# Kernel optimization log

Hardware: AMD Instinct MI355X
Metric: run time of the kernel (lower is better)

The kernel has to match this reference:

```python
import jax, jax.numpy as jnp
import numpy as np

M_DIM = 1024
N_HEADS = 16
H_DIM = M_DIM // N_HEADS
B, S_DEC, S_ENC = 2, 2048, 2048
NEG = -1e9
LN_EPS = 1e-5


def _layernorm(x, g, b):
    mu = jnp.mean(x, axis=-1, keepdims=True)
    var = jnp.mean(jnp.square(x - mu), axis=-1, keepdims=True)
    return (x - mu) * jax.lax.rsqrt(var + LN_EPS) * g + b


def _mha(q_in, kv_in, Wq, bq, Wk, bk, Wv, bv, causal):
    # Wq/Wk/Wv: [H, m_dim, h_dim]; stacked equivalent of per-head nn.Linear
    q = jnp.einsum('bsm,hmd->bhsd', q_in, Wq) + bq[:, None, :]
    k = jnp.einsum('bsm,hmd->bhsd', kv_in, Wk) + bk[:, None, :]
    v = jnp.einsum('bsm,hmd->bhsd', kv_in, Wv) + bv[:, None, :]
    scores = jnp.einsum('bhqd,bhkd->bhqk', q, k) / jnp.sqrt(jnp.asarray(H_DIM, q.dtype))
    if causal:
        sq, sk = scores.shape[-2], scores.shape[-1]
        mask = jnp.tril(jnp.ones((sq, sk), dtype=bool))
        scores = jnp.where(mask, scores, jnp.asarray(NEG, scores.dtype))
    attn = jax.nn.softmax(scores, axis=-1)
    o = jnp.einsum('bhqk,bhkd->bhqd', attn, v)
    bsz, h, sq, d = o.shape
    # concat order: head-major along last dim, same as torch.cat over heads
    return o.transpose(0, 2, 1, 3).reshape(bsz, sq, h * d)


def setup_inputs() -> dict:
    key = jax.random.key(0)
    ks = jax.random.split(key, 32)
    s = 1.0 / np.sqrt(M_DIM)
    s2 = 1.0 / np.sqrt(2 * M_DIM)
    d = {
        'input': jax.random.normal(ks[0], (B, S_DEC, M_DIM), jnp.float32),
        'encoder_out': jax.random.normal(ks[1], (B, S_ENC, M_DIM), jnp.float32),
        # self-attention heads (stacked)
        'Wq1': jax.random.normal(ks[2], (N_HEADS, M_DIM, H_DIM), jnp.float32) * s,
        'bq1': jnp.zeros((N_HEADS, H_DIM), jnp.float32),
        'Wk1': jax.random.normal(ks[3], (N_HEADS, M_DIM, H_DIM), jnp.float32) * s,
        'bk1': jnp.zeros((N_HEADS, H_DIM), jnp.float32),
        'Wv1': jax.random.normal(ks[4], (N_HEADS, M_DIM, H_DIM), jnp.float32) * s,
        'bv1': jnp.zeros((N_HEADS, H_DIM), jnp.float32),
        'Wo1': jax.random.normal(ks[5], (M_DIM, M_DIM), jnp.float32) * s,
        'bo1': jnp.zeros((M_DIM,), jnp.float32),
        'ln1_g': jnp.ones((M_DIM,), jnp.float32),
        'ln1_b': jnp.zeros((M_DIM,), jnp.float32),
        # cross-attention heads (stacked)
        'Wq2': jax.random.normal(ks[6], (N_HEADS, M_DIM, H_DIM), jnp.float32) * s,
        'bq2': jnp.zeros((N_HEADS, H_DIM), jnp.float32),
        'Wk2': jax.random.normal(ks[7], (N_HEADS, M_DIM, H_DIM), jnp.float32) * s,
        'bk2': jnp.zeros((N_HEADS, H_DIM), jnp.float32),
        'Wv2': jax.random.normal(ks[8], (N_HEADS, M_DIM, H_DIM), jnp.float32) * s,
        'bv2': jnp.zeros((N_HEADS, H_DIM), jnp.float32),
        'Wo2': jax.random.normal(ks[9], (M_DIM, M_DIM), jnp.float32) * s,
        'bo2': jnp.zeros((M_DIM,), jnp.float32),
        'ln2_g': jnp.ones((M_DIM,), jnp.float32),
        'ln2_b': jnp.zeros((M_DIM,), jnp.float32),
        # FFN (expansion factor 2, per source)
        'W_ff1': jax.random.normal(ks[10], (M_DIM, 2 * M_DIM), jnp.float32) * s,
        'b_ff1': jnp.zeros((2 * M_DIM,), jnp.float32),
        'W_ff2': jax.random.normal(ks[11], (2 * M_DIM, M_DIM), jnp.float32) * s2,
        'b_ff2': jnp.zeros((M_DIM,), jnp.float32),
        'ln3_g': jnp.ones((M_DIM,), jnp.float32),
        'ln3_b': jnp.zeros((M_DIM,), jnp.float32),
    }
    return d


def reference(input, encoder_out,
              Wq1, bq1, Wk1, bk1, Wv1, bv1, Wo1, bo1, ln1_g, ln1_b,
              Wq2, bq2, Wk2, bk2, Wv2, bv2, Wo2, bo2, ln2_g, ln2_b,
              W_ff1, b_ff1, W_ff2, b_ff2, ln3_g, ln3_b):
    # masked self-attention (dropout = identity in eval)
    sa = _mha(input, input, Wq1, bq1, Wk1, bk1, Wv1, bv1, causal=True)
    sa = sa @ Wo1 + bo1
    out1 = _layernorm(sa + input, ln1_g, ln1_b)
    # cross-attention
    ca = _mha(out1, encoder_out, Wq2, bq2, Wk2, bk2, Wv2, bv2, causal=False)
    ca = ca @ Wo2 + bo2
    out1 = _layernorm(out1 + ca, ln2_g, ln2_b)
    # FFN
    ff = jax.nn.relu(out1 @ W_ff1 + b_ff1) @ W_ff2 + b_ff2
    out = _layernorm(ff + out1, ln3_g, ln3_b)
    return out
```

## Files before the change

### kernel.cpp

```cpp
#include <hip/hip_runtime.h>
#include <math.h>

#define B_ 2
#define S_ 2048
#define M_ 1024
#define H_ 16
#define D_ 64
#define R_ (B_*S_)

typedef __attribute__((ext_vector_type(8))) short short8v;
typedef __attribute__((ext_vector_type(4))) float float4v;
typedef __attribute__((ext_vector_type(16))) float float16v;

__device__ __forceinline__ float4 ld4(const float* p) {
    return *(const float4* __restrict__)p;
}

__device__ __forceinline__ ushort f2bf(float f) {
    union { float f; unsigned u; } x; x.f = f;
    unsigned u = x.u + 0x7fffu + ((x.u >> 16) & 1u);
    return (ushort)(u >> 16);
}
__device__ __forceinline__ float bf2f(ushort s) {
    union { unsigned u; float f; } x; x.u = ((unsigned)s) << 16; return x.f;
}
__device__ __forceinline__ unsigned cvtpk(float lo, float hi) {
    unsigned r;
    asm("v_cvt_pk_bf16_f32 %0, %1, %2" : "=v"(r) : "v"(lo), "v"(hi));
    return r;
}
#if __has_builtin(__builtin_amdgcn_exp2f)
__device__ __forceinline__ float fexp2(float x) { return __builtin_amdgcn_exp2f(x); }
#else
__device__ __forceinline__ float fexp2(float x) { return exp2f(x); }
#endif
#if __has_builtin(__builtin_amdgcn_rcpf)
__device__ __forceinline__ float frcp(float x) { return __builtin_amdgcn_rcpf(x); }
#else
__device__ __forceinline__ float frcp(float x) { return 1.f / x; }
#endif
__device__ __forceinline__ float4v mfma16(short8v a, short8v b, float4v c) {
    return __builtin_amdgcn_mfma_f32_16x16x32_bf16(a, b, c, 0, 0, 0);
}
__device__ __forceinline__ float16v mfma32(short8v a, short8v b, float16v c) {
    return __builtin_amdgcn_mfma_f32_32x32x16_bf16(a, b, c, 0, 0, 0);
}
__device__ __forceinline__ void glds16(const void* g, void* l) {
    __builtin_amdgcn_global_load_lds(
        (const __attribute__((address_space(1))) void*)g,
        (__attribute__((address_space(3))) void*)l, 16, 0, 0);
}

__global__ __launch_bounds__(256) void cast2_k(const float* __restrict__ a,
                                               const float* __restrict__ b,
                                               ushort* __restrict__ oa,
                                               ushort* __restrict__ ob) {
    size_t u = (size_t)blockIdx.x * 256 + threadIdx.x;
    const float* in; ushort* out;
    if (u < (1u << 20)) { in = a; out = oa; }
    else { u -= (1u << 20); in = b; out = ob; }
    float4 v = ld4(in + u * 4);
    ushort4 o = { f2bf(v.x), f2bf(v.y), f2bf(v.z), f2bf(v.w) };
    *(ushort4*)&out[u * 4] = o;
}

__global__ __launch_bounds__(256) void biasp_k(
    const float* __restrict__ q1, const float* __restrict__ k1,
    const float* __restrict__ v1, const float* __restrict__ k2,
    const float* __restrict__ v2, const float* __restrict__ q2,
    float* __restrict__ dst, float SCv) {
    const int seg = blockIdx.x >> 2;
    const int li = (blockIdx.x & 3) * 256 + threadIdx.x;
    const float* s; int off; float sc;
    switch (seg) {
        case 0: s = q1; off = 0;    sc = SCv; break;
        case 1: s = k1; off = 1024; sc = 1.f; break;
        case 2: s = v1; off = 2048; sc = 1.f; break;
        case 3: s = k2; off = 4096; sc = 1.f; break;
        case 4: s = v2; off = 5120; sc = 1.f; break;
        default: s = q2; off = 8192; sc = SCv; break;
    }
    dst[off + li] = s[li] * sc;
}

__global__ __launch_bounds__(256) void wtransH_k(
    const float* __restrict__ s0, const float* __restrict__ s1,
    const float* __restrict__ s2, const float* __restrict__ s3,
    const float* __restrict__ s4, const float* __restrict__ s5,
    ushort* __restrict__ oQKV1, ushort* __restrict__ oQ2,
    ushort* __restrict__ oKV2, float SCv) {
    __shared__ float t[32][33];
    const int z = blockIdx.z, s6 = z >> 4, h = z & 15;
    const float* srcs[6] = { s0, s1, s2, s3, s4, s5 };
    const float* ib = srcs[s6] + (size_t)h * 1024 * 64;
    ushort* ob;
    if (s6 < 3)       ob = oQKV1 + (size_t)s6 * (1024 * 1024) + (size_t)h * (64 * 1024);
    else if (s6 == 3) ob = oQ2 + (size_t)h * (64 * 1024);
    else              ob = oKV2 + (size_t)(s6 - 4) * (1024 * 1024) + (size_t)h * (64 * 1024);
    const float scale = (s6 == 0 || s6 == 3) ? SCv : 1.f;
    const int k0 = blockIdx.y * 32, n0 = blockIdx.x * 32;
    const int tx = threadIdx.x & 31, ty = threadIdx.x >> 5;
    #pragma unroll
    for (int i = 0; i < 4; ++i)
        t[ty + i * 8][tx] = ib[(size_t)(k0 + ty + i * 8) * 64 + n0 + tx];
    __syncthreads();
    #pragma unroll
    for (int i = 0; i < 4; ++i)
        ob[(size_t)(n0 + ty + i * 8) * 1024 + k0 + tx] = f2bf(t[tx][ty + i * 8] * scale);
}

__global__ __launch_bounds__(256) void wtrans_k(const float* __restrict__ inA,
                                                const float* __restrict__ inB,
                                                ushort* __restrict__ outA,
                                                ushort* __restrict__ outB,
                                                int K, int N) {
    __shared__ float t[32][33];
    const float* ib = blockIdx.z ? inB : inA;
    ushort* ob = blockIdx.z ? outB : outA;
    const int k0 = blockIdx.y * 32, n0 = blockIdx.x * 32;
    const int tx = threadIdx.x & 31, ty = threadIdx.x >> 5;
    #pragma unroll
    for (int i = 0; i < 4; ++i)
        t[ty + i * 8][tx] = ib[(size_t)(k0 + ty + i * 8) * N + n0 + tx];
    __syncthreads();
    #pragma unroll
    for (int i = 0; i < 4; ++i)
        ob[(size_t)(n0 + ty + i * 8) * K + k0 + tx] = f2bf(t[tx][ty + i * 8]);
}

template<int TM, int TN, int BK, int OUTMODE, int ACT>
__global__ __launch_bounds__(256) void gemm_bf16_k(
    const ushort* __restrict__ A, const ushort* __restrict__ Bt,
    const float* __restrict__ bias, void* __restrict__ C,
    ushort* __restrict__ Cvt, int matV, int N, int K)
{
    constexpr int NI = TM / 32;
    constexpr int NJ = TN / 32;
    constexpr int KS = BK / 32;
    constexpr int CHR = BK / 8;
    __shared__ __align__(16) ushort At[TM * BK];
    __shared__ __align__(16) ushort Bts[TN * BK];
    const int tid = threadIdx.x, lane = tid & 63, w = tid >> 6;
    const int wm = w >> 1, wn = w & 1;
    const int q = lane & 15, g = lane >> 4;
    const int m0 = blockIdx.y * TM, n0 = blockIdx.x * TN;

    float4v acc[NI][NJ];
    #pragma unroll
    for (int i = 0; i < NI; ++i)
        #pragma unroll
        for (int j = 0; j < NJ; ++j) acc[i][j] = (float4v){0.f, 0.f, 0.f, 0.f};

    for (int k0 = 0; k0 < K; k0 += BK) {
        #pragma unroll
        for (int t = 0; t < TM * CHR / 256; ++t) {
            const int cb = (w * (TM * CHR / 256) + t) * 64;
            const int c = cb + lane;
            const int row = c / CHR, kc = (c % CHR) ^ (row & (CHR - 1));
            glds16(&A[(size_t)(m0 + row) * K + k0 + kc * 8], &At[cb * 8]);
        }
        #pragma unroll
        for (int t = 0; t < TN * CHR / 256; ++t) {
            const int cb = (w * (TN * CHR / 256) + t) * 64;
            const int c = cb + lane;
            const int row = c / CHR, kc = (c % CHR) ^ (row & (CHR - 1));
            glds16(&Bt[(size_t)(n0 + row) * K + k0 + kc * 8], &Bts[cb * 8]);
        }
        __syncthreads();
        #pragma unroll
        for (int ks = 0; ks < KS; ++ks) {
            short8v af[NI], bf[NJ];
            #pragma unroll
            for (int i = 0; i < NI; ++i) {
                const int row = wm * (TM / 2) + i * 16 + q;
                af[i] = *(const short8v*)((const char*)At +
                        row * (BK * 2) + (((ks * 4 + g) ^ (q & (CHR - 1))) << 4));
            }
            #pragma unroll
            for (int j = 0; j < NJ; ++j) {
                const int row = wn * (TN / 2) + j * 16 + q;
                bf[j] = *(const short8v*)((const char*)Bts +
                        row * (BK * 2) + (((ks * 4 + g) ^ (q & (CHR - 1))) << 4));
            }
            #pragma unroll
            for (int i = 0; i < NI; ++i)
                #pragma unroll
                for (int j = 0; j < NJ; ++j)
                    acc[i][j] = mfma16(af[i], bf[j], acc[i][j]);
        }
        __syncthreads();
    }

    float bcol[NJ];
    #pragma unroll
    for (int j = 0; j < NJ; ++j) bcol[j] = bias[n0 + wn * (TN / 2) + j * 16 + q];

    #pragma unroll
    for (int i = 0; i < NI; ++i) {
        const int rowg0 = m0 + wm * (TM / 2) + i * 16 + g * 4;
        #pragma unroll
        for (int j = 0; j < NJ; ++j) {
            const int colg = n0 + wn * (TN / 2) + j * 16 + q;
            float v[4];
            #pragma unroll
            for (int r = 0; r < 4; ++r) {
                v[r] = acc[i][j][r] + bcol[j];
                if (ACT) v[r] = fmaxf(v[r], 0.f);
            }
            if (OUTMODE == 0) {
                #pragma unroll
                for (int r = 0; r < 4; ++r)
                    ((float*)C)[(size_t)(rowg0 + r) * N + colg] = v[r];
            } else if (OUTMODE == 1) {
                #pragma unroll
                for (int r = 0; r < 4; ++r)
                    ((ushort*)C)[(size_t)(rowg0 + r) * N + colg] = f2bf(v[r]);
            } else {
                const int mat = colg >> 10, h = (colg >> 6) & 15, d = colg & 63;
                const int bb = rowg0 >> 11, s0 = rowg0 & 2047;
                if (mat == matV) {
                    uint2 pv;
                    pv.x = cvtpk(v[0], v[1]);
                    pv.y = cvtpk(v[2], v[3]);
                    *(uint2*)&Cvt[((size_t)(bb * H_ + h) * D_ + d) * S_ + s0] = pv;
                } else {
                    #pragma unroll
                    for (int r = 0; r < 4; ++r)
                        ((ushort*)C)[((((size_t)(mat * B_ + bb) * H_ + h) * S_) + s0 + r) * D_ + d] = f2bf(v[r]);
                }
            }
        }
    }
}

template<int CAUSAL>
__global__ __launch_bounds__(256, 3) void fattn_k(
    const ushort* __restrict__ Qg, const ushort* __restrict__ Kg,
    const ushort* __restrict__ VTg, ushort* __restrict__ Og, int Skv)
{
    __shared__ __align__(16) ushort Kt[2][64 * 64];
    __shared__ __align__(16) ushort Vt[2][64 * 64];
    const int tid = threadIdx.x, lane = tid & 63, w = tid >> 6;
    const int q = lane & 31, hi = lane >> 5;
    const int id = blockIdx.x;
    const int bh = id & 31;
    const int t_ = id >> 5;
    const int qb = CAUSAL ? ((t_ < 8) ? (15 - t_) : (t_ - 8)) : t_;
    const int q0b = qb * 128;
    const int q0w = q0b + w * 32;

    const int c0 = tid, c1 = tid + 256;
    const ushort* kS0 = Kg + ((size_t)bh * Skv + (c0 >> 3)) * 64 + (((c0 & 7) ^ ((c0 >> 3) & 7)) * 8);
    const ushort* kS1 = Kg + ((size_t)bh * Skv + (c1 >> 3)) * 64 + (((c1 & 7) ^ ((c1 >> 3) & 7)) * 8);
    const ushort* vS0 = VTg + ((size_t)bh * 64 + (c0 >> 3)) * (size_t)Skv + (((c0 & 7) ^ ((c0 >> 3) & 7)) * 8);
    const ushort* vS1 = VTg + ((size_t)bh * 64 + (c1 >> 3)) * (size_t)Skv + (((c1 & 7) ^ ((c1 >> 3) & 7)) * 8);

#define STAGE(nb) do { \
        glds16(kS0, &Kt[nb][(w * 64) * 8]); \
        glds16(kS1, &Kt[nb][(256 + w * 64) * 8]); \
        glds16(vS0, &Vt[nb][(w * 64) * 8]); \
        glds16(vS1, &Vt[nb][(256 + w * 64) * 8]); \
        kS0 += 64 * 64; kS1 += 64 * 64; vS0 += 64; vS1 += 64; } while (0)

    short8v qf[4];
    #pragma unroll
    for (int ki = 0; ki < 4; ++ki)
        qf[ki] = *(const short8v*)&Qg[((size_t)bh * S_ + q0w + q) * 64 + ki * 16 + hi * 8];

    const int ktB = q * 128 + ((hi ^ (q & 7)) << 4);

    float16v oacc0, oacc1;
    #pragma unroll
    for (int r = 0; r < 16; ++r) { oacc0[r] = 0.f; oacc1[r] = 0.f; }
    float m_ = -1e30f, l_ = 0.f;

    const int ktiles = CAUSAL ? (2 * qb + 2) : (Skv >> 6);
    int cur = 0;

    STAGE(0);
    __syncthreads();

    for (int kt = 0; kt < ktiles; ++kt) {
        if (kt + 1 < ktiles) STAGE(cur ^ 1);
        const char* ktp = (const char*)Kt + cur * 8192;
        const char* vtp = (const char*)Vt + cur * 8192;
        const int kv0 = kt * 64;

        float16v st0, st1;
        #pragma unroll
        for (int r = 0; r < 16; ++r) { st0[r] = 0.f; st1[r] = 0.f; }
        __builtin_amdgcn_s_setprio(1);
        #pragma unroll
        for (int ki = 0; ki < 4; ++ki) {
            short8v kf0 = *(const short8v*)(ktp + (ktB ^ (ki << 5)));
            short8v kf1 = *(const short8v*)(ktp + (ktB ^ (ki << 5)) + 4096);
            st0 = mfma32(kf0, qf[ki], st0);
            st1 = mfma32(kf1, qf[ki], st1);
        }
        __builtin_amdgcn_s_setprio(0);

        if (CAUSAL && kv0 + 63 > q0b) {
            const int qg_ = q0w + q;
            #pragma unroll
            for (int r = 0; r < 16; ++r) {
                const int row = (r & 3) + 8 * (r >> 2) + 4 * hi;
                if (kv0 + row > qg_)      st0[r] = -1e9f;
                if (kv0 + 32 + row > qg_) st1[r] = -1e9f;
            }
        }

        float tm[16];
        #pragma unroll
        for (int r = 0; r < 16; ++r) tm[r] = fmaxf(st0[r], st1[r]);
        #pragma unroll
        for (int off = 8; off >= 1; off >>= 1)
            #pragma unroll
            for (int i = 0; i < 8; ++i)
                if (i < off) tm[i] = fmaxf(tm[i], tm[i + off]);
        float mx = fmaxf(tm[0], __shfl_xor(tm[0], 32));

        if (!__all(mx <= m_)) {
            const float nm = fmaxf(m_, mx);
            const float f = fexp2(m_ - nm);
            l_ *= f;
            oacc0 = oacc0 * f;
            oacc1 = oacc1 * f;
            m_ = nm;
        }

        float ts[16];
        #pragma unroll
        for (int r = 0; r < 16; ++r) {
            st0[r] = fexp2(st0[r] - m_);
            st1[r] = fexp2(st1[r] - m_);
            ts[r] = st0[r] + st1[r];
        }
        #pragma unroll
        for (int off = 8; off >= 1; off >>= 1)
            #pragma unroll
            for (int i = 0; i < 8; ++i)
                if (i < off) ts[i] += ts[i + off];
        l_ += ts[0] + __shfl_xor(ts[0], 32);

        unsigned W0[8], W1[8];
        #pragma unroll
        for (int s = 0; s < 8; ++s) {
            W0[s] = cvtpk(st0[2 * s], st0[2 * s + 1]);
            W1[s] = cvtpk(st1[2 * s], st1[2 * s + 1]);
        }

        short8v bq[4];
        #pragma unroll
        for (int kb = 0; kb < 4; ++kb) {
            union { unsigned u[4]; short8v v; } bb;
            #pragma unroll
            for (int j = 0; j < 4; ++j) {
                const unsigned* Wb = (kb >> 1) ? W1 : W0;
                const int s0 = (j & 1) + 4 * (kb & 1);
                const unsigned own  = hi ? Wb[s0 + 2] : Wb[s0];
                const unsigned send = hi ? Wb[s0]     : Wb[s0 + 2];
                const unsigned rec  = (unsigned)__shfl_xor((int)send, 32);
                bb.u[j] = (j >> 1) ? (hi ? own : rec) : (hi ? rec : own);
            }
            bq[kb] = bb.v;
        }

        __builtin_amdgcn_s_setprio(1);
        #pragma unroll
        for (int kb = 0; kb < 4; ++kb) {
            short8v vf0 = *(const short8v*)(vtp + (ktB ^ (kb << 5)));
            short8v vf1 = *(const short8v*)(vtp + (ktB ^ (kb << 5)) + 4096);
            oacc0 = mfma32(vf0, bq[kb], oacc0);
            oacc1 = mfma32(vf1, bq[kb], oacc1);
        }
        __builtin_amdgcn_s_setprio(0);

        __syncthreads();
        cur ^= 1;
    }
#undef STAGE

    const float inv = frcp(l_);
    char* Ob = (char*)Kt;
    const int qr = w * 32 + q;
    #pragma unroll
    for (int s = 0; s < 8; ++s) {
        const int d0a = 2 * (s & 1) + 8 * (s >> 1) + 4 * hi;
        unsigned wa = cvtpk(oacc0[2 * s] * inv, oacc0[2 * s + 1] * inv);
        *(unsigned*)(Ob + qr * 128 + ((((d0a >> 3) ^ (qr & 7)) << 4) | ((2 * d0a) & 15))) = wa;
        const int d0b = d0a + 32;
        unsigned wb = cvtpk(oacc1[2 * s] * inv, oacc1[2 * s + 1] * inv);
        *(unsigned*)(Ob + qr * 128 + ((((d0b >> 3) ^ (qr & 7)) << 4) | ((2 * d0b) & 15))) = wb;
    }
    __syncthreads();
    const int b = bh >> 4, h = bh & 15;
    #pragma unroll
    for (int t = 0; t < 4; ++t) {
        const int c = t * 256 + tid;
        const int qrow = c >> 3, ch = c & 7;
        short8v v = *(const short8v*)(Ob + qrow * 128 + ((ch ^ (qrow & 7)) << 4));
        *(short8v*)&Og[((size_t)(b * S_ + q0b + qrow)) * M_ + h * 64 + ch * 8] = v;
    }
}

template<int EMITB>
__global__ __launch_bounds__(256) void ln_k(
    const ushort* __restrict__ X, const float* __restrict__ Rz,
    const float* __restrict__ g, const float* __restrict__ be,
    float* __restrict__ outf, ushort* __restrict__ outb)
{
    __shared__ float red[8];
    const int row = blockIdx.x, tid = threadIdx.x;
    const int lane = tid & 63, w = tid >> 6;

    ushort4 xu = *(const ushort4*)&X[(size_t)row * M_ + tid * 4];
    float4 rr = ld4(Rz + (size_t)row * M_ + tid * 4);
    float4 x = make_float4(bf2f(xu.x) + rr.x, bf2f(xu.y) + rr.y,
                           bf2f(xu.z) + rr.z, bf2f(xu.w) + rr.w);

    float sm = x.x + x.y + x.z + x.w;
    #pragma unroll
    for (int off = 1; off < 64; off <<= 1) sm += __shfl_xor(sm, off);
    if (lane == 0) red[w] = sm;
    __syncthreads();
    const float mean = (red[0] + red[1] + red[2] + red[3]) * (1.f / M_);

    x.x -= mean; x.y -= mean; x.z -= mean; x.w -= mean;
    float vs = x.x * x.x + x.y * x.y + x.z * x.z + x.w * x.w;
    #pragma unroll
    for (int off = 1; off < 64; off <<= 1) vs += __shfl_xor(vs, off);
    if (lane == 0) red[4 + w] = vs;
    __syncthreads();
    const float var = (red[4] + red[5] + red[6] + red[7]) * (1.f / M_);
    const float rs = rsqrtf(var + 1e-5f);

    float4 gg = ld4(g + tid * 4), bb = ld4(be + tid * 4);
    float4 y = make_float4(x.x * rs * gg.x + bb.x, x.y * rs * gg.y + bb.y,
                           x.z * rs * gg.z + bb.z, x.w * rs * gg.w + bb.w);
    *(float4*)(outf + (size_t)row * M_ + tid * 4) = y;
    if (EMITB) {
        ushort4 ob = { f2bf(y.x), f2bf(y.y), f2bf(y.z), f2bf(y.w) };
        *(ushort4*)&outb[(size_t)row * M_ + tid * 4] = ob;
    }
}

extern "C" void kernel_launch(void* const* d_in, const int* in_sizes, int n_in,
                              void* d_out, int out_size, void* d_ws, size_t ws_size,
                              hipStream_t stream)
{
    const float* input = (const float*)d_in[0];
    const float* enc   = (const float*)d_in[1];
    const float* Wq1 = (const float*)d_in[2];  const float* bq1 = (const float*)d_in[3];
    const float* Wk1 = (const float*)d_in[4];  const float* bk1 = (const float*)d_in[5];
    const float* Wv1 = (const float*)d_in[6];  const float* bv1 = (const float*)d_in[7];
    const float* Wo1 = (const float*)d_in[8];  const float* bo1 = (const float*)d_in[9];
    const float* ln1g = (const float*)d_in[10]; const float* ln1b = (const float*)d_in[11];
    const float* Wq2 = (const float*)d_in[12]; const float* bq2 = (const float*)d_in[13];
    const float* Wk2 = (const float*)d_in[14]; const float* bk2 = (const float*)d_in[15];
    const float* Wv2 = (const float*)d_in[16]; const float* bv2 = (const float*)d_in[17];
    const float* Wo2 = (const float*)d_in[18]; const float* bo2 = (const float*)d_in[19];
    const float* ln2g = (const float*)d_in[20]; const float* ln2b = (const float*)d_in[21];
    const float* Wf1 = (const float*)d_in[22]; const float* bf1 = (const float*)d_in[23];
    const float* Wf2 = (const float*)d_in[24]; const float* bf2 = (const float*)d_in[25];
    const float* ln3g = (const float*)d_in[26]; const float* ln3b = (const float*)d_in[27];

    const float SC = 0.18033688011112042f;

    char* W = (char*)d_ws;
    #define OFS(mb) ((void*)(W + (size_t)(mb) * 1024 * 1024))
    ushort* x0b    = (ushort*)OFS(0);
    ushort* encb   = (ushort*)OFS(8);
    ushort* WqkvT1 = (ushort*)OFS(16);
    ushort* Wo1T   = (ushort*)OFS(22);
    ushort* Wq2T   = (ushort*)OFS(24);
    ushort* WkvT2  = (ushort*)OFS(26);
    ushort* Wo2T   = (ushort*)OFS(30);
    ushort* Wf1T   = (ushort*)OFS(32);
    ushort* Wf2T   = (ushort*)OFS(36);
    float*  biasQKV1 = (float*)OFS(40);
    float*  biasKV2  = (float*)((char*)OFS(40) + 16384);
    float*  biasQ2   = (float*)((char*)OFS(40) + 32768);
    ushort* QKV1   = (ushort*)OFS(41);
    ushort* VT1    = (ushort*)OFS(65);
    ushort* att1b  = (ushort*)OFS(73);
    ushort* o1b    = (ushort*)OFS(81);
    float*  out1f  = (float*)OFS(41);
    ushort* out1b  = (ushort*)OFS(57);
    ushort* Q2     = (ushort*)OFS(65);
    ushort* KV2    = (ushort*)OFS(73);
    ushort* VT2    = (ushort*)OFS(0);
    ushort* att2b  = (ushort*)OFS(8);
    ushort* o2b    = (ushort*)OFS(65);
    float*  out2f  = (float*)OFS(73);
    ushort* out2b  = (ushort*)OFS(0);
    ushort* ff1b   = (ushort*)OFS(41);
    ushort* ff2b   = (ushort*)OFS(57);
    float*  out    = (float*)d_out;
    const size_t MAT = (size_t)B_ * H_ * S_ * D_;

    dim3 blk(256);

    cast2_k<<<8192, blk, 0, stream>>>(input, enc, x0b, encb);
    biasp_k<<<24, blk, 0, stream>>>(bq1, bk1, bv1, bk2, bv2, bq2, biasQKV1, SC);
    wtransH_k<<<dim3(2, 32, 96), blk, 0, stream>>>(Wq1, Wk1, Wv1, Wq2, Wk2, Wv2,
                                                   WqkvT1, Wq2T, WkvT2, SC);
    wtrans_k<<<dim3(32, 32, 2), blk, 0, stream>>>(Wo1, Wo2, Wo1T, Wo2T, 1024, 1024);
    wtrans_k<<<dim3(64, 32, 1), blk, 0, stream>>>(Wf1, Wf1, Wf1T, Wf1T, 1024, 2048);
    wtrans_k<<<dim3(32, 64, 1), blk, 0, stream>>>(Wf2, Wf2, Wf2T, Wf2T, 2048, 1024);

    gemm_bf16_k<128, 128, 64, 2, 0><<<dim3(24, 32), blk, 0, stream>>>(
        x0b, WqkvT1, biasQKV1, QKV1, VT1, 2, 3072, 1024);
    fattn_k<1><<<dim3(512), blk, 0, stream>>>(QKV1, QKV1 + MAT, VT1, att1b, S_);
    gemm_bf16_k<64, 64, 64, 1, 0><<<dim3(16, 64), blk, 0, stream>>>(
        att1b, Wo1T, bo1, o1b, nullptr, 9, 1024, 1024);
    ln_k<1><<<dim3(R_), blk, 0, stream>>>(o1b, input, ln1g, ln1b, out1f, out1b);

    gemm_bf16_k<64, 64, 64, 2, 0><<<dim3(16, 64), blk, 0, stream>>>(
        out1b, Wq2T, biasQ2, Q2, nullptr, 9, 1024, 1024);
    gemm_bf16_k<128, 128, 64, 2, 0><<<dim3(16, 32), blk, 0, stream>>>(
        encb, WkvT2, biasKV2, KV2, VT2, 1, 2048, 1024);
    fattn_k<0><<<dim3(512), blk, 0, stream>>>(Q2, KV2, VT2, att2b, S_);
    gemm_bf16_k<64, 64, 64, 1, 0><<<dim3(16, 64), blk, 0, stream>>>(
        att2b, Wo2T, bo2, o2b, nullptr, 9, 1024, 1024);
    ln_k<1><<<dim3(R_), blk, 0, stream>>>(o2b, out1f, ln2g, ln2b, out2f, out2b);

    gemm_bf16_k<128, 64, 64, 1, 1><<<dim3(32, 32), blk, 0, stream>>>(
        out2b, Wf1T, bf1, ff1b, nullptr, 9, 2048, 1024);
    gemm_bf16_k<64, 64, 64, 1, 0><<<dim3(16, 64), blk, 0, stream>>>(
        ff1b, Wf2T, bf2, ff2b, nullptr, 9, 1024, 2048);
    ln_k<0><<<dim3(R_), blk, 0, stream>>>(ff2b, out2f, ln3g, ln3b, out, nullptr);
    #undef OFS
}
```

Measured before the change: 315.7 us.

## Restructure flash attention into single-wave blocks with 32-key tiles

Flash attention now runs as single-wavefront blocks, each owning 32 query rows and staging 32-key K/V tiles through its own double-buffered LDS. The grid grows from 512 to 2048 blocks. Barriers are replaced by explicit vmcnt waits, and the causal mask is applied only on the last tile. The aim is to remove cross-wave __syncthreads stalls and improve causal load balance with finer-grained blocks. In exchange, K/V tiles are no longer shared across the four waves, so global and L2 traffic per query rises and each tile iteration does less MFMA work relative to softmax overhead.

```diff
diff --git a/kernel.cpp b/kernel.cpp
--- a/kernel.cpp
+++ b/kernel.cpp
@@ -234,88 +234,91 @@
 }
 
 template<int CAUSAL>
-__global__ __launch_bounds__(256, 3) void fattn_k(
+__global__ __launch_bounds__(64, 2) void fattn_k(
     const ushort* __restrict__ Qg, const ushort* __restrict__ Kg,
     const ushort* __restrict__ VTg, ushort* __restrict__ Og, int Skv)
 {
-    __shared__ __align__(16) ushort Kt[2][64 * 64];
-    __shared__ __align__(16) ushort Vt[2][64 * 64];
-    const int tid = threadIdx.x, lane = tid & 63, w = tid >> 6;
+    __shared__ __align__(16) ushort Kb[2][32 * 64];
+    __shared__ __align__(16) ushort Vb[2][64 * 32];
+    const int lane = threadIdx.x;
     const int q = lane & 31, hi = lane >> 5;
     const int id = blockIdx.x;
     const int bh = id & 31;
     const int t_ = id >> 5;
-    const int qb = CAUSAL ? ((t_ < 8) ? (15 - t_) : (t_ - 8)) : t_;
-    const int q0b = qb * 128;
-    const int q0w = q0b + w * 32;
-
-    const int c0 = tid, c1 = tid + 256;
-    const ushort* kS0 = Kg + ((size_t)bh * Skv + (c0 >> 3)) * 64 + (((c0 & 7) ^ ((c0 >> 3) & 7)) * 8);
-    const ushort* kS1 = Kg + ((size_t)bh * Skv + (c1 >> 3)) * 64 + (((c1 & 7) ^ ((c1 >> 3) & 7)) * 8);
-    const ushort* vS0 = VTg + ((size_t)bh * 64 + (c0 >> 3)) * (size_t)Skv + (((c0 & 7) ^ ((c0 >> 3) & 7)) * 8);
-    const ushort* vS1 = VTg + ((size_t)bh * 64 + (c1 >> 3)) * (size_t)Skv + (((c1 & 7) ^ ((c1 >> 3) & 7)) * 8);
+    const int qb = CAUSAL ? (63 - t_) : t_;
+    const int q0w = qb * 32;
+
+    const ushort* kS[4]; const ushort* vS[4];
+    #pragma unroll
+    for (int i = 0; i < 4; ++i) {
+        const int c = i * 64 + lane;
+        const int rk = c >> 3, chk = c & 7;
+        kS[i] = Kg + ((size_t)bh * Skv + rk) * 64 + ((chk ^ (rk & 7)) * 8);
+        const int rv = c >> 2, chv = c & 3;
+        vS[i] = VTg + ((size_t)bh * 64 + rv) * (size_t)Skv + ((chv ^ ((rv >> 1) & 3)) * 8);
+    }
 
 #define STAGE(nb) do { \
-        glds16(kS0, &Kt[nb][(w * 64) * 8]); \
-        glds16(kS1, &Kt[nb][(256 + w * 64) * 8]); \
-        glds16(vS0, &Vt[nb][(w * 64) * 8]); \
-        glds16(vS1, &Vt[nb][(256 + w * 64) * 8]); \
-        kS0 += 64 * 64; kS1 += 64 * 64; vS0 += 64; vS1 += 64; } while (0)
+        glds16(kS[0], &Kb[nb][0]);    glds16(kS[1], &Kb[nb][512]); \
+        glds16(kS[2], &Kb[nb][1024]); glds16(kS[3], &Kb[nb][1536]); \
+        glds16(vS[0], &Vb[nb][0]);    glds16(vS[1], &Vb[nb][512]); \
+        glds16(vS[2], &Vb[nb][1024]); glds16(vS[3], &Vb[nb][1536]); \
+        kS[0] += 32 * 64; kS[1] += 32 * 64; kS[2] += 32 * 64; kS[3] += 32 * 64; \
+        vS[0] += 32; vS[1] += 32; vS[2] += 32; vS[3] += 32; } while (0)
 
     short8v qf[4];
     #pragma unroll
     for (int ki = 0; ki < 4; ++ki)
         qf[ki] = *(const short8v*)&Qg[((size_t)bh * S_ + q0w + q) * 64 + ki * 16 + hi * 8];
 
-    const int ktB = q * 128 + ((hi ^ (q & 7)) << 4);
-
     float16v oacc0, oacc1;
     #pragma unroll
     for (int r = 0; r < 16; ++r) { oacc0[r] = 0.f; oacc1[r] = 0.f; }
     float m_ = -1e30f, l_ = 0.f;
 
-    const int ktiles = CAUSAL ? (2 * qb + 2) : (Skv >> 6);
+    const int T = CAUSAL ? (qb + 1) : (Skv >> 5);
     int cur = 0;
 
     STAGE(0);
-    __syncthreads();
-
-    for (int kt = 0; kt < ktiles; ++kt) {
-        if (kt + 1 < ktiles) STAGE(cur ^ 1);
-        const char* ktp = (const char*)Kt + cur * 8192;
-        const char* vtp = (const char*)Vt + cur * 8192;
-        const int kv0 = kt * 64;
-
-        float16v st0, st1;
-        #pragma unroll
-        for (int r = 0; r < 16; ++r) { st0[r] = 0.f; st1[r] = 0.f; }
+
+    for (int kt = 0; kt < T; ++kt) {
+        if (kt + 1 < T) {
+            STAGE(cur ^ 1);
+            asm volatile("s_waitcnt vmcnt(8)" ::: "memory");
+        } else {
+            asm volatile("s_waitcnt vmcnt(0)" ::: "memory");
+        }
+        const ushort* kb = Kb[cur];
+        const ushort* vb = Vb[cur];
+        const int kv0 = kt * 32;
+
+        float16v st;
+        #pragma unroll
+        for (int r = 0; r < 16; ++r) st[r] = 0.f;
         __builtin_amdgcn_s_setprio(1);
         #pragma unroll
         for (int ki = 0; ki < 4; ++ki) {
-            short8v kf0 = *(const short8v*)(ktp + (ktB ^ (ki << 5)));
-            short8v kf1 = *(const short8v*)(ktp + (ktB ^ (ki << 5)) + 4096);
-            st0 = mfma32(kf0, qf[ki], st0);
-            st1 = mfma32(kf1, qf[ki], st1);
+            short8v kfr = *(const short8v*)((const char*)kb +
+                          q * 128 + (((2 * ki + hi) ^ (q & 7)) << 4));
+            st = mfma32(kfr, qf[ki], st);
         }
         __builtin_amdgcn_s_setprio(0);
 
-        if (CAUSAL && kv0 + 63 > q0b) {
-            const int qg_ = q0w + q;
+        if (CAUSAL && kt == T - 1) {
             #pragma unroll
             for (int r = 0; r < 16; ++r) {
                 const int row = (r & 3) + 8 * (r >> 2) + 4 * hi;
-                if (kv0 + row > qg_)      st0[r] = -1e9f;
-                if (kv0 + 32 + row > qg_) st1[r] = -1e9f;
+                if (kv0 + row > q0w + q) st[r] = -1e9f;
             }
         }
 
-        float tm[16];
-        #pragma unroll
-        for (int r = 0; r < 16; ++r) tm[r] = fmaxf(st0[r], st1[r]);
-        #pragma unroll
-        for (int off = 8; off >= 1; off >>= 1)
-            #pragma unroll
-            for (int i = 0; i < 8; ++i)
+        float tm[8];
+        #pragma unroll
+        for (int i = 0; i < 8; ++i) tm[i] = fmaxf(st[i], st[i + 8]);
+        #pragma unroll
+        for (int off = 4; off >= 1; off >>= 1)
+            #pragma unroll
+            for (int i = 0; i < 4; ++i)
                 if (i < off) tm[i] = fmaxf(tm[i], tm[i + off]);
         float mx = fmaxf(tm[0], __shfl_xor(tm[0], 32));
 
@@ -328,78 +331,72 @@
             m_ = nm;
         }
 
-        float ts[16];
-        #pragma unroll
-        for (int r = 0; r < 16; ++r) {
-            st0[r] = fexp2(st0[r] - m_);
-            st1[r] = fexp2(st1[r] - m_);
-            ts[r] = st0[r] + st1[r];
-        }
-        #pragma unroll
-        for (int off = 8; off >= 1; off >>= 1)
-            #pragma unroll
-            for (int i = 0; i < 8; ++i)
+        float ts[8];
+        #pragma unroll
+        for (int r = 0; r < 16; ++r) st[r] = fexp2(st[r] - m_);
+        #pragma unroll
+        for (int i = 0; i < 8; ++i) ts[i] = st[i] + st[i + 8];
+        #pragma unroll
+        for (int off = 4; off >= 1; off >>= 1)
+            #pragma unroll
+            for (int i = 0; i < 4; ++i)
                 if (i < off) ts[i] += ts[i + off];
         l_ += ts[0] + __shfl_xor(ts[0], 32);
 
-        unsigned W0[8], W1[8];
-        #pragma unroll
-        for (int s = 0; s < 8; ++s) {
-            W0[s] = cvtpk(st0[2 * s], st0[2 * s + 1]);
-            W1[s] = cvtpk(st1[2 * s], st1[2 * s + 1]);
-        }
-
-        short8v bq[4];
-        #pragma unroll
-        for (int kb = 0; kb < 4; ++kb) {
+        unsigned W[8];
+        #pragma unroll
+        for (int s = 0; s < 8; ++s) W[s] = cvtpk(st[2 * s], st[2 * s + 1]);
+
+        short8v bq[2];
+        #pragma unroll
+        for (int kb2 = 0; kb2 < 2; ++kb2) {
             union { unsigned u[4]; short8v v; } bb;
             #pragma unroll
             for (int j = 0; j < 4; ++j) {
-                const unsigned* Wb = (kb >> 1) ? W1 : W0;
-                const int s0 = (j & 1) + 4 * (kb & 1);
-                const unsigned own  = hi ? Wb[s0 + 2] : Wb[s0];
-                const unsigned send = hi ? Wb[s0]     : Wb[s0 + 2];
+                const int s0 = (j & 1) + 4 * kb2;
+                const unsigned own  = hi ? W[s0 + 2] : W[s0];
+                const unsigned send = hi ? W[s0]     : W[s0 + 2];
                 const unsigned rec  = (unsigned)__shfl_xor((int)send, 32);
                 bb.u[j] = (j >> 1) ? (hi ? own : rec) : (hi ? rec : own);
             }
-            bq[kb] = bb.v;
+            bq[kb2] = bb.v;
         }
 
         __builtin_amdgcn_s_setprio(1);
         #pragma unroll
-        for (int kb = 0; kb < 4; ++kb) {
-            short8v vf0 = *(const short8v*)(vtp + (ktB ^ (kb << 5)));
-            short8v vf1 = *(const short8v*)(vtp + (ktB ^ (kb << 5)) + 4096);
-            oacc0 = mfma32(vf0, bq[kb], oacc0);
-            oacc1 = mfma32(vf1, bq[kb], oacc1);
+        for (int kb2 = 0; kb2 < 2; ++kb2) {
+            const int x = 2 * kb2 + hi;
+            short8v vf0 = *(const short8v*)((const char*)vb +
+                          q * 64 + ((x ^ ((q >> 1) & 3)) << 4));
+            short8v vf1 = *(const short8v*)((const char*)vb +
+                          (32 + q) * 64 + ((x ^ (((32 + q) >> 1) & 3)) << 4));
+            oacc0 = mfma32(vf0, bq[kb2], oacc0);
+            oacc1 = mfma32(vf1, bq[kb2], oacc1);
         }
         __builtin_amdgcn_s_setprio(0);
 
-        __syncthreads();
         cur ^= 1;
     }
 #undef STAGE
 
     const float inv = frcp(l_);
-    char* Ob = (char*)Kt;
-    const int qr = w * 32 + q;
+    char* Ob = (char*)Kb[0];
     #pragma unroll
     for (int s = 0; s < 8; ++s) {
         const int d0a = 2 * (s & 1) + 8 * (s >> 1) + 4 * hi;
         unsigned wa = cvtpk(oacc0[2 * s] * inv, oacc0[2 * s + 1] * inv);
-        *(unsigned*)(Ob + qr * 128 + ((((d0a >> 3) ^ (qr & 7)) << 4) | ((2 * d0a) & 15))) = wa;
+        *(unsigned*)(Ob + q * 128 + ((((d0a >> 3) ^ (q & 7)) << 4) | ((2 * d0a) & 15))) = wa;
         const int d0b = d0a + 32;
         unsigned wb = cvtpk(oacc1[2 * s] * inv, oacc1[2 * s + 1] * inv);
-        *(unsigned*)(Ob + qr * 128 + ((((d0b >> 3) ^ (qr & 7)) << 4) | ((2 * d0b) & 15))) = wb;
-    }
-    __syncthreads();
+        *(unsigned*)(Ob + q * 128 + ((((d0b >> 3) ^ (q & 7)) << 4) | ((2 * d0b) & 15))) = wb;
+    }
     const int b = bh >> 4, h = bh & 15;
     #pragma unroll
     for (int t = 0; t < 4; ++t) {
-        const int c = t * 256 + tid;
+        const int c = t * 64 + lane;
         const int qrow = c >> 3, ch = c & 7;
         short8v v = *(const short8v*)(Ob + qrow * 128 + ((ch ^ (qrow & 7)) << 4));
-        *(short8v*)&Og[((size_t)(b * S_ + q0b + qrow)) * M_ + h * 64 + ch * 8] = v;
+        *(short8v*)&Og[((size_t)(b * S_ + q0w + qrow)) * M_ + h * 64 + ch * 8] = v;
     }
 }
 
@@ -499,6 +496,7 @@
     const size_t MAT = (size_t)B_ * H_ * S_ * D_;
 
     dim3 blk(256);
+    dim3 blkW(64);
 
     cast2_k<<<8192, blk, 0, stream>>>(input, enc, x0b, encb);
     biasp_k<<<24, blk, 0, stream>>>(bq1, bk1, bv1, bk2, bv2, bq2, biasQKV1, SC);
@@ -510,7 +508,7 @@
 
     gemm_bf16_k<128, 128, 64, 2, 0><<<dim3(24, 32), blk, 0, stream>>>(
         x0b, WqkvT1, biasQKV1, QKV1, VT1, 2, 3072, 1024);
-    fattn_k<1><<<dim3(512), blk, 0, stream>>>(QKV1, QKV1 + MAT, VT1, att1b, S_);
+    fattn_k<1><<<dim3(2048), blkW, 0, stream>>>(QKV1, QKV1 + MAT, VT1, att1b, S_);
     gemm_bf16_k<64, 64, 64, 1, 0><<<dim3(16, 64), blk, 0, stream>>>(
         att1b, Wo1T, bo1, o1b, nullptr, 9, 1024, 1024);
     ln_k<1><<<dim3(R_), blk, 0, stream>>>(o1b, input, ln1g, ln1b, out1f, out1b);
@@ -519,7 +517,7 @@
         out1b, Wq2T, biasQ2, Q2, nullptr, 9, 1024, 1024);
     gemm_bf16_k<128, 128, 64, 2, 0><<<dim3(16, 32), blk, 0, stream>>>(
         encb, WkvT2, biasKV2, KV2, VT2, 1, 2048, 1024);
-    fattn_k<0><<<dim3(512), blk, 0, stream>>>(Q2, KV2, VT2, att2b, S_);
+    fattn_k<0><<<dim3(2048), blkW, 0, stream>>>(Q2, KV2, VT2, att2b, S_);
     gemm_bf16_k<64, 64, 64, 1, 0><<<dim3(16, 64), blk, 0, stream>>>(
         att2b, Wo2T, bo2, o2b, nullptr, 9, 1024, 1024);
     ln_k<1><<<dim3(R_), blk, 0, stream>>>(o2b, out1f, ln2g, ln2b, out2f, out2b);
```

After: 360.4 us. 14.2% more time.
